# Kernel tuning notes

Hardware: AMD Instinct MI355X
Metric: run time of the kernel (lower is better)

## Reference

```python
import jax, jax.numpy as jnp
import numpy as np

P = 30           # max_pad_size
S = 224          # image_size
CROP = S - 2 * P # 164
B = 16
T = 16


def _interp1d(out_pos, in_size, out_size, base):
    """PyTorch bilinear (align_corners=False) 1D source indices/weights.
    out_pos: float32 positions local to the region; out_size: traced int scalar;
    in_size: static python int; base: static offset into a concatenated source.
    Returns (i0, i1, w) with i0,i1 in [base, base+in_size).
    """
    scale = jnp.float32(in_size) / out_size.astype(jnp.float32)
    f = jnp.maximum((out_pos + 0.5) * scale - 0.5, 0.0)
    i0 = jnp.floor(f).astype(jnp.int32)
    w = f - i0.astype(jnp.float32)
    i1 = jnp.minimum(i0 + 1, in_size - 1)
    return i0 + base, i1 + base, w


def _make_prompt(pu, pd, pl, pr, off_r, off_d):
    # pu [3,2P,S], pd [3,P,S], pl [3,CROP,2P], pr [3,CROP,P]
    off_l = 2 * P - off_r
    off_u = 2 * P - off_d

    # ---- horizontal: build middle rows [3, CROP, S] = [pad_left | zeros | pad_right]
    j = jnp.arange(S, dtype=jnp.int32)
    jf = j.astype(jnp.float32)
    src_h = jnp.concatenate([pl, pr], axis=-1)  # [3, CROP, 3P]
    i0l, i1l, wl = _interp1d(jf, 2 * P, off_l, 0)
    i0r, i1r, wr = _interp1d(jf - (S - off_r).astype(jnp.float32), P, off_r, 2 * P)
    mL = j < off_l
    mR = j >= S - off_r
    idx0 = jnp.where(mL, i0l, i0r)
    idx1 = jnp.where(mL, i1l, i1r)
    w = jnp.where(mL, wl, wr)
    mid = src_h[:, :, idx0] * (1.0 - w) + src_h[:, :, idx1] * w
    mid = jnp.where((mL | mR)[None, None, :], mid, 0.0)  # [3, CROP, S]

    # ---- vertical: [pad_up ; mid ; pad_down] -> [3, S, S]
    cat_v = jnp.concatenate([pu, pd, mid], axis=1)  # [3, 3P+CROP, S]
    i = jnp.arange(S, dtype=jnp.int32)
    if_ = i.astype(jnp.float32)
    i0u, i1u, wu = _interp1d(if_, 2 * P, off_u, 0)
    i0d, i1d, wd = _interp1d(if_ - (S - off_d).astype(jnp.float32), P, off_d, 2 * P)
    mid_idx = i - off_u + 3 * P  # middle rows copied verbatim (weight 0)
    mU = i < off_u
    mD = i >= S - off_d
    r0 = jnp.where(mU, i0u, jnp.where(mD, i0d, mid_idx))
    r1 = jnp.where(mU, i1u, jnp.where(mD, i1d, mid_idx))
    wv = jnp.where(mU, wu, jnp.where(mD, wd, 0.0))
    return cat_v[:, r0, :] * (1.0 - wv)[None, :, None] + cat_v[:, r1, :] * wv[None, :, None]


def setup_inputs() -> dict:
    key = jax.random.key(0)
    ks = jax.random.split(key, 8)
    x = jax.random.normal(ks[0], (B, 3, T, S, S), dtype=jnp.float32)
    pad_up = jax.random.normal(ks[1], (3, 3, 2 * P, S), dtype=jnp.float32)
    pad_down = jax.random.normal(ks[2], (3, 3, P, S), dtype=jnp.float32)
    pad_left = jax.random.normal(ks[3], (3, 3, CROP, 2 * P), dtype=jnp.float32)
    pad_right = jax.random.normal(ks[4], (3, 3, CROP, P), dtype=jnp.float32)
    cam_views = jax.random.randint(ks[5], (B,), 0, 3, dtype=jnp.int32)
    offsets_right = jax.random.randint(ks[6], (B,), 1, P + 1, dtype=jnp.int32)
    offsets_down = jax.random.randint(ks[7], (B,), 1, P + 1, dtype=jnp.int32)
    return {"x": x, "pad_up": pad_up, "pad_down": pad_down, "pad_left": pad_left,
            "pad_right": pad_right, "cam_views": cam_views,
            "offsets_right": offsets_right, "offsets_down": offsets_down}


def reference(x, pad_up, pad_down, pad_left, pad_right, cam_views, offsets_right, offsets_down):
    def per_sample(cam, orr, od):
        return _make_prompt(pad_up[cam], pad_down[cam], pad_left[cam], pad_right[cam], orr, od)

    prompt = jax.vmap(per_sample)(cam_views, offsets_right, offsets_down)  # [B,3,S,S]
    return x + prompt[:, :, None, :, :]  # broadcast over T frames
```

## Files before the change

### kernel.cpp

```cpp
#include <hip/hip_runtime.h>


#define PP 30
#define SS 224
#define CROPC 164
#define BB 16
#define TT 16

__device__ __forceinline__ void interp1d(float pos, float in_size, int in_size_i,
                                         int out_size, int& i0, int& i1, float& w) {
    float scale = in_size / (float)out_size;
    float f = fmaxf((pos + 0.5f) * scale - 0.5f, 0.0f);
    i0 = (int)floorf(f);
    w = f - (float)i0;
    i1 = min(i0 + 1, in_size_i - 1);
}

__global__ void __launch_bounds__(256)
prompt_build_kernel(const float* __restrict__ pu,
                    const float* __restrict__ pd,
                    const float* __restrict__ pl,
                    const float* __restrict__ pr,
                    const int* __restrict__ cam_views,
                    const int* __restrict__ offs_r,
                    const int* __restrict__ offs_d,
                    float* __restrict__ prompt) {
    const int J4 = SS / 4;
    int idx = blockIdx.x * blockDim.x + threadIdx.x;
    const int total = BB * 3 * SS * J4;
    if (idx >= total) return;

    int j4 = idx % J4;
    int tmp = idx / J4;
    int i = tmp % SS;
    tmp /= SS;
    int c = tmp % 3;
    int b = tmp / 3;

    const int cam = cam_views[b];
    const int off_r = offs_r[b];
    const int off_d = offs_d[b];
    const int off_l = 2 * PP - off_r;
    const int off_u = 2 * PP - off_d;

    const float* puc = pu + (size_t)(cam * 3 + c) * (2 * PP) * SS;
    const float* pdc = pd + (size_t)(cam * 3 + c) * PP * SS;
    const float* plc = pl + (size_t)(cam * 3 + c) * CROPC * (2 * PP);
    const float* prc = pr + (size_t)(cam * 3 + c) * CROPC * PP;

    const int j0 = j4 * 4;
    float pv[4];

    if (i < off_u) {
        int r0, r1; float w;
        interp1d((float)i, (float)(2 * PP), 2 * PP, off_u, r0, r1, w);
        const float* a = puc + (size_t)r0 * SS + j0;
        const float* bp = puc + (size_t)r1 * SS + j0;
        #pragma unroll
        for (int k = 0; k < 4; k++)
            pv[k] = a[k] * (1.0f - w) + bp[k] * w;
    } else if (i >= SS - off_d) {
        int r0, r1; float w;
        interp1d((float)(i - (SS - off_d)), (float)PP, PP, off_d, r0, r1, w);
        const float* a = pdc + (size_t)r0 * SS + j0;
        const float* bp = pdc + (size_t)r1 * SS + j0;
        #pragma unroll
        for (int k = 0; k < 4; k++)
            pv[k] = a[k] * (1.0f - w) + bp[k] * w;
    } else {
        const int r = i - off_u;
        const float* plr = plc + (size_t)r * (2 * PP);
        const float* prr = prc + (size_t)r * PP;
        #pragma unroll
        for (int k = 0; k < 4; k++) {
            int j = j0 + k;
            float v = 0.0f;
            if (j < off_l) {
                int c0, c1; float w;
                interp1d((float)j, (float)(2 * PP), 2 * PP, off_l, c0, c1, w);
                v = plr[c0] * (1.0f - w) + plr[c1] * w;
            } else if (j >= SS - off_r) {
                int c0, c1; float w;
                interp1d((float)(j - (SS - off_r)), (float)PP, PP, off_r, c0, c1, w);
                v = prr[c0] * (1.0f - w) + prr[c1] * w;
            }
            pv[k] = v;
        }
    }

    float4 o; o.x = pv[0]; o.y = pv[1]; o.z = pv[2]; o.w = pv[3];
    *reinterpret_cast<float4*>(prompt + (size_t)idx * 4) = o;
}

__global__ void __launch_bounds__(256)
stream_add_kernel(const float* __restrict__ x,
                  const float* __restrict__ prompt,
                  float* __restrict__ out) {
    const int P4 = SS * SS / 4;
    int idx = blockIdx.x * blockDim.x + threadIdx.x;
    int p4 = idx % P4;
    int frame = idx / P4;
    int bc = frame / TT;

    const float4 xv = *reinterpret_cast<const float4*>(x + (size_t)idx * 4);
    const float4 pv = *reinterpret_cast<const float4*>(prompt + ((size_t)bc * P4 + p4) * 4);
    float4 ov;
    ov.x = xv.x + pv.x;
    ov.y = xv.y + pv.y;
    ov.z = xv.z + pv.z;
    ov.w = xv.w + pv.w;
    *reinterpret_cast<float4*>(out + (size_t)idx * 4) = ov;
}

__global__ void __launch_bounds__(256)
fused_kernel(const float* __restrict__ x,
             const float* __restrict__ pu, const float* __restrict__ pd,
             const float* __restrict__ pl, const float* __restrict__ pr,
             const int* __restrict__ cam_views,
             const int* __restrict__ offs_r, const int* __restrict__ offs_d,
             float* __restrict__ out) {
    const int J4 = SS / 4;
    int idx = blockIdx.x * blockDim.x + threadIdx.x;
    const int total = BB * 3 * SS * J4;
    if (idx >= total) return;
    int j4 = idx % J4;
    int tmp = idx / J4;
    int i = tmp % SS;
    tmp /= SS;
    int c = tmp % 3;
    int b = tmp / 3;
    const int cam = cam_views[b];
    const int off_r = offs_r[b];
    const int off_d = offs_d[b];
    const int off_l = 2 * PP - off_r;
    const int off_u = 2 * PP - off_d;
    const float* puc = pu + (size_t)(cam * 3 + c) * (2 * PP) * SS;
    const float* pdc = pd + (size_t)(cam * 3 + c) * PP * SS;
    const float* plc = pl + (size_t)(cam * 3 + c) * CROPC * (2 * PP);
    const float* prc = pr + (size_t)(cam * 3 + c) * CROPC * PP;
    const int j0 = j4 * 4;
    float pv[4];
    if (i < off_u) {
        int r0, r1; float w;
        interp1d((float)i, (float)(2 * PP), 2 * PP, off_u, r0, r1, w);
        const float* a = puc + (size_t)r0 * SS + j0;
        const float* bp = puc + (size_t)r1 * SS + j0;
        #pragma unroll
        for (int k = 0; k < 4; k++) pv[k] = a[k] * (1.0f - w) + bp[k] * w;
    } else if (i >= SS - off_d) {
        int r0, r1; float w;
        interp1d((float)(i - (SS - off_d)), (float)PP, PP, off_d, r0, r1, w);
        const float* a = pdc + (size_t)r0 * SS + j0;
        const float* bp = pdc + (size_t)r1 * SS + j0;
        #pragma unroll
        for (int k = 0; k < 4; k++) pv[k] = a[k] * (1.0f - w) + bp[k] * w;
    } else {
        const int r = i - off_u;
        const float* plr = plc + (size_t)r * (2 * PP);
        const float* prr = prc + (size_t)r * PP;
        #pragma unroll
        for (int k = 0; k < 4; k++) {
            int j = j0 + k;
            float v = 0.0f;
            if (j < off_l) {
                int c0, c1; float w;
                interp1d((float)j, (float)(2 * PP), 2 * PP, off_l, c0, c1, w);
                v = plr[c0] * (1.0f - w) + plr[c1] * w;
            } else if (j >= SS - off_r) {
                int c0, c1; float w;
                interp1d((float)(j - (SS - off_r)), (float)PP, PP, off_r, c0, c1, w);
                v = prr[c0] * (1.0f - w) + prr[c1] * w;
            }
            pv[k] = v;
        }
    }
    size_t base = ((size_t)(b * 3 + c) * TT) * (SS * SS) + (size_t)i * SS + j0;
    #pragma unroll
    for (int t = 0; t < TT; t++) {
        size_t off = base + (size_t)t * (SS * SS);
        float4 xv = *reinterpret_cast<const float4*>(x + off);
        float4 ov;
        ov.x = xv.x + pv[0]; ov.y = xv.y + pv[1];
        ov.z = xv.z + pv[2]; ov.w = xv.w + pv[3];
        *reinterpret_cast<float4*>(out + off) = ov;
    }
}

extern "C" void kernel_launch(void* const* d_in, const int* in_sizes, int n_in,
                              void* d_out, int out_size, void* d_ws, size_t ws_size,
                              hipStream_t stream) {
    const float* x  = (const float*)d_in[0];
    const float* pu = (const float*)d_in[1];
    const float* pd = (const float*)d_in[2];
    const float* pl = (const float*)d_in[3];
    const float* pr = (const float*)d_in[4];
    const int* cam  = (const int*)d_in[5];
    const int* orr  = (const int*)d_in[6];
    const int* od   = (const int*)d_in[7];
    float* out = (float*)d_out;

    const size_t prompt_bytes = (size_t)BB * 3 * SS * SS * sizeof(float);

    if (ws_size >= prompt_bytes) {
        float* prompt = (float*)d_ws;
        const int total_p = BB * 3 * SS * (SS / 4);
        prompt_build_kernel<<<(total_p + 255) / 256, 256, 0, stream>>>(
            pu, pd, pl, pr, cam, orr, od, prompt);
        const int total_s = BB * 3 * TT * SS * (SS / 4);
        stream_add_kernel<<<(total_s + 255) / 256, 256, 0, stream>>>(x, prompt, out);
    } else {
        const int total = BB * 3 * SS * (SS / 4);
        fused_kernel<<<(total + 255) / 256, 256, 0, stream>>>(
            x, pu, pd, pl, pr, cam, orr, od, out);
    }
}
```

Baseline: 271.2 us.

## Fuse prompt build into streaming add with 4-frame groups and nontemporal IO

Replaces the two-kernel path (build the prompt into the workspace, then stream x + prompt) with one kernel. Each thread computes its prompt values inline and applies them to a group of 4 frames. All 4 frame loads are issued up front, and loads and stores use nontemporal hints. This removes the prompt workspace write and reread and one launch, while keeping more threads than the old 16-frame fused fallback. The cost is that the interpolation is recomputed 4 times per pixel instead of once.

```diff
diff --git a/kernel.cpp b/kernel.cpp
--- a/kernel.cpp
+++ b/kernel.cpp
@@ -6,6 +6,9 @@
 #define CROPC 164
 #define BB 16
 #define TT 16
+#define TGRP 4
+
+typedef float f4 __attribute__((ext_vector_type(4)));
 
 __device__ __forceinline__ void interp1d(float pos, float in_size, int in_size_i,
                                          int out_size, int& i0, int& i1, float& w) {
@@ -17,25 +20,39 @@
 }
 
 __global__ void __launch_bounds__(256)
-prompt_build_kernel(const float* __restrict__ pu,
-                    const float* __restrict__ pd,
-                    const float* __restrict__ pl,
-                    const float* __restrict__ pr,
-                    const int* __restrict__ cam_views,
-                    const int* __restrict__ offs_r,
-                    const int* __restrict__ offs_d,
-                    float* __restrict__ prompt) {
+fused4_kernel(const float* __restrict__ x,
+              const float* __restrict__ pu,
+              const float* __restrict__ pd,
+              const float* __restrict__ pl,
+              const float* __restrict__ pr,
+              const int* __restrict__ cam_views,
+              const int* __restrict__ offs_r,
+              const int* __restrict__ offs_d,
+              float* __restrict__ out) {
     const int J4 = SS / 4;
+    const int NG = TT / TGRP;
     int idx = blockIdx.x * blockDim.x + threadIdx.x;
-    const int total = BB * 3 * SS * J4;
+    const int total = BB * 3 * NG * SS * J4;
     if (idx >= total) return;
 
     int j4 = idx % J4;
     int tmp = idx / J4;
     int i = tmp % SS;
     tmp /= SS;
+    int tg = tmp % NG;
+    tmp /= NG;
     int c = tmp % 3;
     int b = tmp / 3;
+
+    const int j0 = j4 * 4;
+
+    size_t base = (((size_t)(b * 3 + c) * TT + (size_t)tg * TGRP) * (SS * SS))
+                  + (size_t)i * SS + j0;
+    f4 xv[TGRP];
+    #pragma unroll
+    for (int k = 0; k < TGRP; k++)
+        xv[k] = __builtin_nontemporal_load(
+            reinterpret_cast<const f4*>(x + base + (size_t)k * (SS * SS)));
 
     const int cam = cam_views[b];
     const int off_r = offs_r[b];
@@ -48,13 +65,11 @@
     const float* plc = pl + (size_t)(cam * 3 + c) * CROPC * (2 * PP);
     const float* prc = pr + (size_t)(cam * 3 + c) * CROPC * PP;
 
-    const int j0 = j4 * 4;
     float pv[4];
-
     if (i < off_u) {
         int r0, r1; float w;
         interp1d((float)i, (float)(2 * PP), 2 * PP, off_u, r0, r1, w);
-        const float* a = puc + (size_t)r0 * SS + j0;
+        const float* a  = puc + (size_t)r0 * SS + j0;
         const float* bp = puc + (size_t)r1 * SS + j0;
         #pragma unroll
         for (int k = 0; k < 4; k++)
@@ -62,7 +77,7 @@
     } else if (i >= SS - off_d) {
         int r0, r1; float w;
         interp1d((float)(i - (SS - off_d)), (float)PP, PP, off_d, r0, r1, w);
-        const float* a = pdc + (size_t)r0 * SS + j0;
+        const float* a  = pdc + (size_t)r0 * SS + j0;
         const float* bp = pdc + (size_t)r1 * SS + j0;
         #pragma unroll
         for (int k = 0; k < 4; k++)
@@ -88,101 +103,15 @@
         }
     }
 
-    float4 o; o.x = pv[0]; o.y = pv[1]; o.z = pv[2]; o.w = pv[3];
-    *reinterpret_cast<float4*>(prompt + (size_t)idx * 4) = o;
-}
-
-__global__ void __launch_bounds__(256)
-stream_add_kernel(const float* __restrict__ x,
-                  const float* __restrict__ prompt,
-                  float* __restrict__ out) {
-    const int P4 = SS * SS / 4;
-    int idx = blockIdx.x * blockDim.x + threadIdx.x;
-    int p4 = idx % P4;
-    int frame = idx / P4;
-    int bc = frame / TT;
-
-    const float4 xv = *reinterpret_cast<const float4*>(x + (size_t)idx * 4);
-    const float4 pv = *reinterpret_cast<const float4*>(prompt + ((size_t)bc * P4 + p4) * 4);
-    float4 ov;
-    ov.x = xv.x + pv.x;
-    ov.y = xv.y + pv.y;
-    ov.z = xv.z + pv.z;
-    ov.w = xv.w + pv.w;
-    *reinterpret_cast<float4*>(out + (size_t)idx * 4) = ov;
-}
-
-__global__ void __launch_bounds__(256)
-fused_kernel(const float* __restrict__ x,
-             const float* __restrict__ pu, const float* __restrict__ pd,
-             const float* __restrict__ pl, const float* __restrict__ pr,
-             const int* __restrict__ cam_views,
-             const int* __restrict__ offs_r, const int* __restrict__ offs_d,
-             float* __restrict__ out) {
-    const int J4 = SS / 4;
-    int idx = blockIdx.x * blockDim.x + threadIdx.x;
-    const int total = BB * 3 * SS * J4;
-    if (idx >= total) return;
-    int j4 = idx % J4;
-    int tmp = idx / J4;
-    int i = tmp % SS;
-    tmp /= SS;
-    int c = tmp % 3;
-    int b = tmp / 3;
-    const int cam = cam_views[b];
-    const int off_r = offs_r[b];
-    const int off_d = offs_d[b];
-    const int off_l = 2 * PP - off_r;
-    const int off_u = 2 * PP - off_d;
-    const float* puc = pu + (size_t)(cam * 3 + c) * (2 * PP) * SS;
-    const float* pdc = pd + (size_t)(cam * 3 + c) * PP * SS;
-    const float* plc = pl + (size_t)(cam * 3 + c) * CROPC * (2 * PP);
-    const float* prc = pr + (size_t)(cam * 3 + c) * CROPC * PP;
-    const int j0 = j4 * 4;
-    float pv[4];
-    if (i < off_u) {
-        int r0, r1; float w;
-        interp1d((float)i, (float)(2 * PP), 2 * PP, off_u, r0, r1, w);
-        const float* a = puc + (size_t)r0 * SS + j0;
-        const float* bp = puc + (size_t)r1 * SS + j0;
-        #pragma unroll
-        for (int k = 0; k < 4; k++) pv[k] = a[k] * (1.0f - w) + bp[k] * w;
-    } else if (i >= SS - off_d) {
-        int r0, r1; float w;
-        interp1d((float)(i - (SS - off_d)), (float)PP, PP, off_d, r0, r1, w);
-        const float* a = pdc + (size_t)r0 * SS + j0;
-        const float* bp = pdc + (size_t)r1 * SS + j0;
-        #pragma unroll
-        for (int k = 0; k < 4; k++) pv[k] = a[k] * (1.0f - w) + bp[k] * w;
-    } else {
-        const int r = i - off_u;
-        const float* plr = plc + (size_t)r * (2 * PP);
-        const float* prr = prc + (size_t)r * PP;
-        #pragma unroll
-        for (int k = 0; k < 4; k++) {
-            int j = j0 + k;
-            float v = 0.0f;
-            if (j < off_l) {
-                int c0, c1; float w;
-                interp1d((float)j, (float)(2 * PP), 2 * PP, off_l, c0, c1, w);
-                v = plr[c0] * (1.0f - w) + plr[c1] * w;
-            } else if (j >= SS - off_r) {
-                int c0, c1; float w;
-                interp1d((float)(j - (SS - off_r)), (float)PP, PP, off_r, c0, c1, w);
-                v = prr[c0] * (1.0f - w) + prr[c1] * w;
-            }
-            pv[k] = v;
-        }
-    }
-    size_t base = ((size_t)(b * 3 + c) * TT) * (SS * SS) + (size_t)i * SS + j0;
     #pragma unroll
-    for (int t = 0; t < TT; t++) {
-        size_t off = base + (size_t)t * (SS * SS);
-        float4 xv = *reinterpret_cast<const float4*>(x + off);
-        float4 ov;
-        ov.x = xv.x + pv[0]; ov.y = xv.y + pv[1];
-        ov.z = xv.z + pv[2]; ov.w = xv.w + pv[3];
-        *reinterpret_cast<float4*>(out + off) = ov;
+    for (int k = 0; k < TGRP; k++) {
+        f4 ov = xv[k];
+        ov[0] += pv[0];
+        ov[1] += pv[1];
+        ov[2] += pv[2];
+        ov[3] += pv[3];
+        __builtin_nontemporal_store(
+            ov, reinterpret_cast<f4*>(out + base + (size_t)k * (SS * SS)));
     }
 }
 
@@ -199,18 +128,7 @@
     const int* od   = (const int*)d_in[7];
     float* out = (float*)d_out;
 
-    const size_t prompt_bytes = (size_t)BB * 3 * SS * SS * sizeof(float);
-
-    if (ws_size >= prompt_bytes) {
-        float* prompt = (float*)d_ws;
-        const int total_p = BB * 3 * SS * (SS / 4);
-        prompt_build_kernel<<<(total_p + 255) / 256, 256, 0, stream>>>(
-            pu, pd, pl, pr, cam, orr, od, prompt);
-        const int total_s = BB * 3 * TT * SS * (SS / 4);
-        stream_add_kernel<<<(total_s + 255) / 256, 256, 0, stream>>>(x, prompt, out);
-    } else {
-        const int total = BB * 3 * SS * (SS / 4);
-        fused_kernel<<<(total + 255) / 256, 256, 0, stream>>>(
-            x, pu, pd, pl, pr, cam, orr, od, out);
-    }
+    const int total = BB * 3 * (TT / TGRP) * SS * (SS / 4);
+    fused4_kernel<<<(total + 255) / 256, 256, 0, stream>>>(
+        x, pu, pd, pl, pr, cam, orr, od, out);
 }
```

Result: faster. 263.4 us (-2.9%).
